# Kernel optimization log

Measured on AMD Instinct MI355X. Metric: run time of the kernel, lower is better.

Reference implementation:

```python
import jax, jax.numpy as jnp
import numpy as np

N_RAYS = 8192
M = 524288
GX, GY, GZ = 160, 160, 128
NFEAT = 12
POS_PE, VIEW_PE = 10, 4
WIDTH = 128
POS_DIM = 3 + 3 * POS_PE * 2      # 63
VIEW_DIM = 3 + 3 * VIEW_PE * 2    # 27
DIM0 = NFEAT + POS_DIM            # 75
ACT_SHIFT = float(np.log(1.0 / (1.0 - 1e-6) - 1.0))  # density bias shift from alpha_init
INTERVAL = 0.5                    # stepsize * voxel_size_ratio
XYZ_MIN, XYZ_MAX = -1.0, 1.0


def posemb(x, n_pe):
    # x: [N,3] -> [N, 3 + 3*n_pe*2], matching cat([x, sin(x*freq), cos(x*freq)])
    freq = 2.0 ** jnp.arange(n_pe, dtype=x.dtype)
    xf = (x[..., None] * freq).reshape(x.shape[0], -1)
    return jnp.concatenate([x, jnp.sin(xf), jnp.cos(xf)], axis=-1)


def trilinear(grid, xyz):
    # grid: [X,Y,Z,C]; xyz: [M,3] in world coords. align_corners=True bilinear (grid_sample).
    sz_f = jnp.array(grid.shape[:3], jnp.float32)
    sz_i = jnp.array(grid.shape[:3], jnp.int32)
    t = (xyz - XYZ_MIN) / (XYZ_MAX - XYZ_MIN) * (sz_f - 1.0)
    t = jnp.clip(t, 0.0, sz_f - 1.0)
    i0 = jnp.clip(jnp.floor(t).astype(jnp.int32), 0, sz_i - 2)
    f = t - i0.astype(t.dtype)
    out = jnp.zeros((xyz.shape[0], grid.shape[-1]), t.dtype)
    for dx in (0, 1):
        for dy in (0, 1):
            for dz in (0, 1):
                w = ((f[:, 0] if dx else 1.0 - f[:, 0])
                     * (f[:, 1] if dy else 1.0 - f[:, 1])
                     * (f[:, 2] if dz else 1.0 - f[:, 2]))
                out = out + w[:, None] * grid[i0[:, 0] + dx, i0[:, 1] + dy, i0[:, 2] + dz]
    return out


def mask_lookup(mask, xyz):
    # nearest-neighbor maskcache_lookup: ijk = round(xyz*scale + shift)
    sz_f = jnp.array(mask.shape, jnp.float32)
    scale = (sz_f - 1.0) / (XYZ_MAX - XYZ_MIN)
    shift = -XYZ_MIN * scale
    ijk = jnp.clip(jnp.round(xyz * scale + shift).astype(jnp.int32), 0,
                   jnp.array(mask.shape, jnp.int32) - 1)
    return mask[ijk[:, 0], ijk[:, 1], ijk[:, 2]]


def alphas2weights(alpha, ray_id, n_rays):
    # segmented T_i = prod_{j<i in ray}(1-alpha_j); weights = T*alpha (ray_id sorted)
    log1a = jnp.log(jnp.clip(1.0 - alpha, 1e-10, 1.0))
    excl = jnp.cumsum(log1a) - log1a                      # global exclusive cumsum
    seg_tot = jax.ops.segment_sum(log1a, ray_id, num_segments=n_rays)
    seg_start = jnp.cumsum(seg_tot) - seg_tot             # exclusive prefix over rays
    T = jnp.exp(excl - seg_start[ray_id])
    weights = T * alpha
    alphainv_last = jnp.exp(seg_tot)
    return weights, alphainv_last


def setup_inputs() -> dict:
    key = jax.random.key(0)
    ks = jax.random.split(key, 16)
    xyz = jax.random.uniform(ks[0], (M, 3), jnp.float32) * (XYZ_MAX - XYZ_MIN) + XYZ_MIN
    ray_id = jnp.sort(jax.random.randint(ks[1], (M,), 0, N_RAYS))
    viewdirs = jax.random.normal(ks[2], (N_RAYS, 3), jnp.float32)
    viewdirs = viewdirs / jnp.linalg.norm(viewdirs, axis=-1, keepdims=True)
    mask = jax.random.uniform(ks[3], (GX, GY, GZ)) > 0.1
    density = jax.random.normal(ks[4], (GX, GY, GZ), jnp.float32) * 0.5
    k0 = jax.random.normal(ks[5], (GX, GY, GZ, NFEAT), jnp.float32) * 0.1
    s = 0.05
    W0 = jax.random.normal(ks[6], (DIM0, WIDTH), jnp.float32) * s
    b0 = jnp.zeros((WIDTH,), jnp.float32)
    W1 = jax.random.normal(ks[7], (WIDTH, WIDTH), jnp.float32) * s
    b1 = jnp.zeros((WIDTH,), jnp.float32)
    W2 = jax.random.normal(ks[8], (WIDTH, WIDTH), jnp.float32) * s
    b2 = jnp.zeros((WIDTH,), jnp.float32)
    Wr = jax.random.normal(ks[9], (WIDTH + VIEW_DIM, 3), jnp.float32) * s
    br = jnp.zeros((3,), jnp.float32)
    return {"xyz": xyz, "ray_id": ray_id, "viewdirs": viewdirs, "mask": mask,
            "density": density, "k0": k0, "W0": W0, "b0": b0, "W1": W1, "b1": b1,
            "W2": W2, "b2": b2, "Wr": Wr, "br": br}


def reference(xyz, ray_id, viewdirs, mask, density, k0, W0, b0, W1, b1, W2, b2, Wr, br):
    # 1) empty-space skipping via mask cache (kept as multiplicative mask for static shapes)
    m = mask_lookup(mask, xyz).astype(xyz.dtype)
    # 2) trilinear density query + raw2alpha
    d = trilinear(density[..., None], xyz)[:, 0]
    alpha = 1.0 - (1.0 + jnp.exp(d + ACT_SHIFT)) ** (-INTERVAL)
    alpha = alpha * m
    # 3) segmented alpha compositing (Alphas2Weights)
    weights, alphainv_last = alphas2weights(alpha, ray_id, N_RAYS)
    # 4) feature query + view MLP -> rgb
    feat = trilinear(k0, xyz)                              # [M, NFEAT]
    h = jnp.concatenate([feat, posemb(xyz, POS_PE)], -1)   # [M, DIM0]
    h = jax.nn.relu(h @ W0 + b0)
    h = jax.nn.relu(h @ W1 + b1)
    h = jax.nn.relu(h @ W2 + b2)
    ve = posemb(viewdirs, VIEW_PE)[ray_id]                 # [M, VIEW_DIM]
    rgb = jax.nn.sigmoid(jnp.concatenate([h, ve], -1) @ Wr + br)
    # 5) composite per ray + white background
    rgb_marched = jax.ops.segment_sum(weights[:, None] * rgb, ray_id, num_segments=N_RAYS)
    rgb_marched = rgb_marched + alphainv_last[:, None] * 1.0
    return rgb_marched
```

## Files before the change

### kernel.cpp

```cpp
#include <hip/hip_runtime.h>
#include <hip/hip_bf16.h>

#define M_SAMPLES 524288
#define NRAYS 8192
#define GXD 160
#define GYD 160
#define GZD 128
#define GYZ (GYD*GZD)
#define NVOX (GXD*GYD*GZD)
#define ACT_SHIFT -13.81550955796f
#define ROWA 136
#define ROWB 168

typedef __bf16 bf16x8 __attribute__((ext_vector_type(8)));
typedef float f32x4 __attribute__((ext_vector_type(4)));
typedef float f32x16 __attribute__((ext_vector_type(16)));

static __device__ inline unsigned short f2bf(float f){
  __hip_bfloat16 h = __float2bfloat16(f);
  unsigned short u; __builtin_memcpy(&u, &h, 2); return u;
}

#if defined(__has_builtin)
#if __has_builtin(__builtin_amdgcn_cvt_pk_bf16_f32)
#define HAVE_PK_BF16 1
#endif
#endif

static __device__ inline unsigned int packbf(float a, float b){
#ifdef HAVE_PK_BF16
  typedef __bf16 bf16v2 __attribute__((ext_vector_type(2)));
  bf16v2 r = __builtin_amdgcn_cvt_pk_bf16_f32(a, b);
  unsigned int u; __builtin_memcpy(&u, &r, 4); return u;
#else
  return (unsigned int)f2bf(a) | ((unsigned int)f2bf(b) << 16);
#endif
}

struct Tri {
  int ix, iy, iz;
  float wx0, wx1, wy0, wy1, wz0, wz1;
};
static __device__ inline Tri tri_setup(float x, float y, float z){
  Tri t;
  float tx = (x+1.f)*0.5f*(float)(GXD-1); tx = fminf(fmaxf(tx,0.f),(float)(GXD-1));
  float ty = (y+1.f)*0.5f*(float)(GYD-1); ty = fminf(fmaxf(ty,0.f),(float)(GYD-1));
  float tz = (z+1.f)*0.5f*(float)(GZD-1); tz = fminf(fmaxf(tz,0.f),(float)(GZD-1));
  t.ix = min((int)tx, GXD-2); t.iy = min((int)ty, GYD-2); t.iz = min((int)tz, GZD-2);
  float fx = tx-t.ix, fy = ty-t.iy, fz = tz-t.iz;
  t.wx0 = 1.f-fx; t.wx1 = fx; t.wy0 = 1.f-fy; t.wy1 = fy; t.wz0 = 1.f-fz; t.wz1 = fz;
  return t;
}

__global__ void k_detect(const unsigned int* __restrict__ mw, int* __restrict__ flag){
  unsigned int v = mw[threadIdx.x & 63];
  unsigned long long any = __ballot(v > 1u);
  if(threadIdx.x == 0) *flag = (any != 0ull) ? 1 : 0;
}

__global__ __launch_bounds__(256) void k_prep_w(const float* __restrict__ W0,
    const float* __restrict__ W1, const float* __restrict__ W2,
    const float* __restrict__ Wr,
    unsigned short* __restrict__ wt0, unsigned short* __restrict__ wt1,
    unsigned short* __restrict__ wt2, unsigned short* __restrict__ wtr)
{
  int t = blockIdx.x*256 + threadIdx.x;
  if(t < 128*96){
    int n = t/96, k = t%96;
    wt0[t] = f2bf((k < 75) ? W0[k*128 + n] : 0.f);
  } else if(t < 128*96 + 16384){
    int j = t - 128*96; int n = j/128, k = j%128;
    wt1[j] = f2bf(W1[k*128 + n]);
  } else if(t < 128*96 + 32768){
    int j = t - 128*96 - 16384; int n = j/128, k = j%128;
    wt2[j] = f2bf(W2[k*128 + n]);
  } else if(t < 128*96 + 32768 + 16*160){
    int j = t - 128*96 - 32768; int n = j/160, k = j%160;
    wtr[j] = f2bf((n < 3 && k < 155) ? Wr[k*3 + n] : 0.f);
  }
}

__global__ __launch_bounds__(256) void k_viewemb(const float* __restrict__ vd,
                                                 float* __restrict__ ve)
{
  int t = blockIdx.x*256 + threadIdx.x;
  if(t >= NRAYS*27) return;
  int ray = t/27, c = t%27;
  float v;
  if(c < 3) v = vd[ray*3 + c];
  else if(c < 15){
    int q = c - 3; int ci = q/4, p = q%4;
    v = sinf(vd[ray*3 + ci] * (float)(1 << p));
  } else {
    int q = c - 15; int ci = q/4, p = q%4;
    v = cosf(vd[ray*3 + ci] * (float)(1 << p));
  }
  ve[t] = v;
}

template<int KDIM, int SROW, int DROW>
static __device__ inline void layer32(const unsigned short* src, unsigned short* dst,
    const unsigned short* __restrict__ wt, const float* __restrict__ bias,
    int wave, int ln, int kh)
{
  constexpr int NS = KDIM/16;
  int tile_s = wave & 1, tile_n = wave >> 1;
  const unsigned short* wbase = wt + (tile_n*32 + ln)*KDIM + kh*8;
  const unsigned short* abase = src + (tile_s*32 + ln)*SROW + kh*8;
  f32x16 acc = {0.f,0.f,0.f,0.f,0.f,0.f,0.f,0.f,0.f,0.f,0.f,0.f,0.f,0.f,0.f,0.f};
  #pragma unroll
  for(int st = 0; st < NS; ++st){
    bf16x8 af = *(const bf16x8*)(wbase + st*16);
    bf16x8 bfr = *(const bf16x8*)(abase + st*16);
    acc = __builtin_amdgcn_mfma_f32_32x32x16_bf16(af, bfr, acc, 0, 0, 0);
  }
  int scol = tile_s*32 + ln;
  #pragma unroll
  for(int g = 0; g < 4; ++g){
    int n0 = tile_n*32 + g*8 + kh*4;
    float4 bv = *(const float4*)(bias + n0);
    unsigned int lo = packbf(fmaxf(acc[4*g+0] + bv.x, 0.f), fmaxf(acc[4*g+1] + bv.y, 0.f));
    unsigned int hi = packbf(fmaxf(acc[4*g+2] + bv.z, 0.f), fmaxf(acc[4*g+3] + bv.w, 0.f));
    unsigned long long o = (unsigned long long)lo | ((unsigned long long)hi << 32);
    *(unsigned long long*)(dst + scol*DROW + n0) = o;
  }
}

__global__ __launch_bounds__(512) void k_mlp(const float* __restrict__ xyz,
    const float* __restrict__ density, const float* __restrict__ k0,
    const void* __restrict__ mask, const int* __restrict__ flag,
    const int* __restrict__ ray_id,
    const unsigned short* __restrict__ wt0, const unsigned short* __restrict__ wt1,
    const unsigned short* __restrict__ wt2, const unsigned short* __restrict__ wtr,
    const float* __restrict__ b0, const float* __restrict__ b1,
    const float* __restrict__ b2, const float* __restrict__ br,
    const float* __restrict__ ve,
    float* __restrict__ alpha_w, float4* __restrict__ rgb_out)
{
  __shared__ alignas(16) unsigned short hA[64*ROWA];
  __shared__ alignas(16) unsigned short hB[64*ROWB];
  __shared__ float red[64][4];

  int tid = threadIdx.x;
  int lane = tid & 63, wave = tid >> 6;

  if(wave < 4){
    int smp = (wave << 4) | (lane >> 2);
    int corner = lane & 3;
    int i = blockIdx.x*64 + smp;
    float x = xyz[3*i+0], y = xyz[3*i+1], z = xyz[3*i+2];
    Tri t = tri_setup(x, y, z);
    int dx = corner & 1, dy = corner >> 1;
    float wxy = (dx ? t.wx1 : t.wx0) * (dy ? t.wy1 : t.wy0);
    float w0 = wxy*t.wz0, w1 = wxy*t.wz1;
    size_t vox = (size_t)((t.ix+dx)*GYZ + (t.iy+dy)*GZD + t.iz);
    float pd = w0*density[vox] + w1*density[vox+1];
    const float4* v = (const float4*)(k0 + vox*12);
    float4 a0 = v[0], a1 = v[1], a2 = v[2];
    float4 c0 = v[3], c1 = v[4], c2 = v[5];
    float pf[12];
    pf[0] = w0*a0.x + w1*c0.x;  pf[1] = w0*a0.y + w1*c0.y;
    pf[2] = w0*a0.z + w1*c0.z;  pf[3] = w0*a0.w + w1*c0.w;
    pf[4] = w0*a1.x + w1*c1.x;  pf[5] = w0*a1.y + w1*c1.y;
    pf[6] = w0*a1.z + w1*c1.z;  pf[7] = w0*a1.w + w1*c1.w;
    pf[8] = w0*a2.x + w1*c2.x;  pf[9] = w0*a2.y + w1*c2.y;
    pf[10]= w0*a2.z + w1*c2.z;  pf[11]= w0*a2.w + w1*c2.w;
    #pragma unroll
    for(int m2 = 1; m2 < 4; m2 <<= 1){
      pd += __shfl_xor(pd, m2);
      #pragma unroll
      for(int j = 0; j < 12; ++j) pf[j] += __shfl_xor(pf[j], m2);
    }
    if(corner == 0){
      int mx = (int)rintf(x*79.5f + 79.5f); mx = min(max(mx,0), GXD-1);
      int my = (int)rintf(y*79.5f + 79.5f); my = min(max(my,0), GYD-1);
      int mz = (int)rintf(z*63.5f + 63.5f); mz = min(max(mz,0), GZD-1);
      int midx = mx*GYZ + my*GZD + mz;
      bool mm = (*flag) ? (((const unsigned char*)mask)[midx] != 0)
                        : (((const int*)mask)[midx] != 0);
      float e = expf(pd + ACT_SHIFT);
      float alpha = 1.f - rsqrtf(1.f + e);
      if(!mm) alpha = 0.f;
      alpha_w[i] = alpha;
      unsigned int d[8];
      #pragma unroll
      for(int j = 0; j < 6; ++j) d[j] = packbf(pf[2*j], pf[2*j+1]);
      d[6] = packbf(x, y);
      d[7] = packbf(z, __sinf(x));
      uint4* p = (uint4*)(hA + smp*ROWA);
      p[0] = make_uint4(d[0],d[1],d[2],d[3]);
      p[1] = make_uint4(d[4],d[5],d[6],d[7]);
    } else if(corner == 1){
      uint4* p = (uint4*)(hA + smp*ROWA + 80);
      p[0] = make_uint4(0,0,0,0);
      p[1] = make_uint4(0,0,0,0);
    } else {
      int ray = ray_id[i];
      int cb = (corner - 2) * 16;
      unsigned int d[8];
      #pragma unroll
      for(int j = 0; j < 8; ++j){
        int c = cb + 2*j;
        float a = (c     < 27) ? ve[ray*27 + c]     : 0.f;
        float b = (c + 1 < 27) ? ve[ray*27 + c + 1] : 0.f;
        d[j] = packbf(a, b);
      }
      uint4* p = (uint4*)(hB + smp*ROWB + 128 + cb);
      p[0] = make_uint4(d[0],d[1],d[2],d[3]);
      p[1] = make_uint4(d[4],d[5],d[6],d[7]);
    }
  } else {
    int chunk = wave - 3;
    int i2 = blockIdx.x*64 + lane;
    float x = xyz[3*i2+0], y = xyz[3*i2+1], z = xyz[3*i2+2];
    float vv[16];
    #pragma unroll
    for(int j = 0; j < 16; ++j){
      int c = chunk*16 + j;
      float r;
      if(c >= 75) r = 0.f;
      else {
        int q = (c < 45) ? (c-15) : (c-45);
        int ci = q/10, p = q - ci*10;
        float xv = (ci == 0) ? x : ((ci == 1) ? y : z);
        float a = xv * (float)(1 << p);
        r = (c < 45) ? __sinf(a) : __cosf(a);
      }
      vv[j] = r;
    }
    unsigned int d[8];
    #pragma unroll
    for(int j = 0; j < 8; ++j) d[j] = packbf(vv[2*j], vv[2*j+1]);
    uint4* p = (uint4*)(hA + lane*ROWA + chunk*16);
    p[0] = make_uint4(d[0],d[1],d[2],d[3]);
    p[1] = make_uint4(d[4],d[5],d[6],d[7]);
  }
  __syncthreads();

  int ln = lane & 31, kh = lane >> 5;
  layer32< 96, ROWA, ROWB>(hA, hB, wt0, b0, wave, ln, kh);  __syncthreads();
  layer32<128, ROWB, ROWA>(hB, hA, wt1, b1, wave, ln, kh);  __syncthreads();
  layer32<128, ROWA, ROWB>(hA, hB, wt2, b2, wave, ln, kh);  __syncthreads();

  int col = lane & 15, q = lane >> 4;
  if(wave < 4){
    int mt = wave;
    f32x4 acc = {0.f, 0.f, 0.f, 0.f};
    const unsigned short* arow = hB + (mt*16 + col)*ROWB + q*8;
    const unsigned short* wrow = wtr + col*160 + q*8;
    #pragma unroll
    for(int ks = 0; ks < 5; ++ks){
      bf16x8 af = *(const bf16x8*)(arow + ks*32);
      bf16x8 bfr = *(const bf16x8*)(wrow + ks*32);
      acc = __builtin_amdgcn_mfma_f32_16x16x32_bf16(af, bfr, acc, 0, 0, 0);
    }
    if(col < 3){
      #pragma unroll
      for(int r = 0; r < 4; ++r){
        int sl = mt*16 + q*4 + r;
        float v = acc[r] + br[col];
        red[sl][col] = 1.f / (1.f + expf(-v));
      }
    }
  }
  __syncthreads();

  if(wave == 7){
    int i2 = blockIdx.x*64 + lane;
    rgb_out[i2] = make_float4(red[lane][0], red[lane][1], red[lane][2], 0.f);
  }
}

__global__ __launch_bounds__(256) void k_comp2(const int* __restrict__ ray_id,
    const float* __restrict__ alpha_w, const float4* __restrict__ rgb,
    float* __restrict__ out)
{
  int r = blockIdx.x*4 + (threadIdx.x >> 6);
  int lane = threadIdx.x & 63;
  int lo = 0, hi = M_SAMPLES;
  while(lo < hi){ int mid = (lo+hi) >> 1; if(ray_id[mid] < r) lo = mid+1; else hi = mid; }
  int s = lo;
  int lo2 = s, hi2 = M_SAMPLES;
  while(lo2 < hi2){ int mid = (lo2+hi2) >> 1; if(ray_id[mid] < r+1) lo2 = mid+1; else hi2 = mid; }
  int e = lo2;

  float carry = 1.f;
  float ar = 0.f, ag = 0.f, ab = 0.f;
  for(int base = s; base < e; base += 64){
    int idx = base + lane;
    float a = (idx < e) ? alpha_w[idx] : 0.f;
    float incl = 1.f - a;
    #pragma unroll
    for(int d2 = 1; d2 < 64; d2 <<= 1){
      float t = __shfl_up(incl, d2);
      if(lane >= d2) incl *= t;
    }
    float excl = __shfl_up(incl, 1);
    if(lane == 0) excl = 1.f;
    float w = carry * excl * a;
    if(idx < e){
      float4 c = rgb[idx];
      ar += w*c.x; ag += w*c.y; ab += w*c.z;
    }
    carry *= __shfl(incl, 63);
  }
  #pragma unroll
  for(int m2 = 1; m2 < 64; m2 <<= 1){
    ar += __shfl_xor(ar, m2);
    ag += __shfl_xor(ag, m2);
    ab += __shfl_xor(ab, m2);
  }
  if(lane == 0){
    out[3*r+0] = ar + carry;
    out[3*r+1] = ag + carry;
    out[3*r+2] = ab + carry;
  }
}

extern "C" void kernel_launch(void* const* d_in, const int* in_sizes, int n_in,
                              void* d_out, int out_size, void* d_ws, size_t ws_size,
                              hipStream_t stream)
{
  const float* xyz      = (const float*)d_in[0];
  const int*   ray_id   = (const int*)  d_in[1];
  const float* viewdirs = (const float*)d_in[2];
  const void*  mask     =               d_in[3];
  const float* density  = (const float*)d_in[4];
  const float* k0       = (const float*)d_in[5];
  const float* W0 = (const float*)d_in[6];  const float* b0 = (const float*)d_in[7];
  const float* W1 = (const float*)d_in[8];  const float* b1 = (const float*)d_in[9];
  const float* W2 = (const float*)d_in[10]; const float* b2 = (const float*)d_in[11];
  const float* Wr = (const float*)d_in[12]; const float* br = (const float*)d_in[13];
  float* out = (float*)d_out;

  char* ws = (char*)d_ws;
  size_t off = 0;
  auto take = [&](size_t nbytes) -> void* {
    void* p = ws + off;
    off = (off + nbytes + 255) & ~(size_t)255;
    return p;
  };
  int*            flag    = (int*)           take(4);
  unsigned short* wt0     = (unsigned short*)take(128*96*2);
  unsigned short* wt1     = (unsigned short*)take(128*128*2);
  unsigned short* wt2     = (unsigned short*)take(128*128*2);
  unsigned short* wtr     = (unsigned short*)take(16*160*2);
  float*          ve      = (float*)         take((size_t)NRAYS*27*4);
  float*          alpha_w = (float*)         take((size_t)M_SAMPLES*4);
  float4*         rgb_ws  = (float4*)        take((size_t)M_SAMPLES*16);

  k_detect <<<1,   64,  0, stream>>>((const unsigned int*)mask, flag);
  k_prep_w <<<186, 256, 0, stream>>>(W0, W1, W2, Wr, wt0, wt1, wt2, wtr);
  k_viewemb<<<864, 256, 0, stream>>>(viewdirs, ve);
  k_mlp    <<<M_SAMPLES/64, 512, 0, stream>>>(xyz, density, k0, mask, flag,
                                              ray_id, wt0, wt1, wt2, wtr,
                                              b0, b1, b2, br, ve, alpha_w, rgb_ws);
  k_comp2  <<<NRAYS/4, 256, 0, stream>>>(ray_id, alpha_w, rgb_ws, out);
}
```

Before: 488.8 us.

## Repack density and k0 grids into compact FP8 voxel records and merge prep kernels

Adds a per-call repack kernel that interleaves density (fp32) with the 12 k0 features, stored as FP8 in one 16-byte record per voxel (bf16 in 32 bytes as a fallback). The MLP kernel then gathers two packed records per corner instead of separate density and 48-byte feature reads, cutting gather traffic. It also merges the detect, weight-prep and view-embedding kernels into one launch. The trade-off is an extra full-grid pass over roughly 3.3M voxels on every call, and FP8 feature quantization that may exceed tolerance.

```diff
diff --git a/kernel.cpp b/kernel.cpp
--- a/kernel.cpp
+++ b/kernel.cpp
@@ -15,15 +15,21 @@
 typedef __bf16 bf16x8 __attribute__((ext_vector_type(8)));
 typedef float f32x4 __attribute__((ext_vector_type(4)));
 typedef float f32x16 __attribute__((ext_vector_type(16)));
+typedef float f32v2 __attribute__((ext_vector_type(2)));
 
 static __device__ inline unsigned short f2bf(float f){
   __hip_bfloat16 h = __float2bfloat16(f);
   unsigned short u; __builtin_memcpy(&u, &h, 2); return u;
 }
+static __device__ inline float flo(unsigned int u){ return __uint_as_float(u << 16); }
+static __device__ inline float fhi(unsigned int u){ return __uint_as_float(u & 0xffff0000u); }
 
 #if defined(__has_builtin)
 #if __has_builtin(__builtin_amdgcn_cvt_pk_bf16_f32)
 #define HAVE_PK_BF16 1
+#endif
+#if __has_builtin(__builtin_amdgcn_cvt_pk_f32_fp8) && __has_builtin(__builtin_amdgcn_cvt_pk_fp8_f32)
+#define HAVE_FP8 1
 #endif
 #endif
 
@@ -52,38 +58,39 @@
   return t;
 }
 
-__global__ void k_detect(const unsigned int* __restrict__ mw, int* __restrict__ flag){
-  unsigned int v = mw[threadIdx.x & 63];
-  unsigned long long any = __ballot(v > 1u);
-  if(threadIdx.x == 0) *flag = (any != 0ull) ? 1 : 0;
-}
-
-__global__ __launch_bounds__(256) void k_prep_w(const float* __restrict__ W0,
-    const float* __restrict__ W1, const float* __restrict__ W2,
-    const float* __restrict__ Wr,
+__global__ __launch_bounds__(256) void k_prep(const unsigned int* __restrict__ mw,
+    int* __restrict__ flag,
+    const float* __restrict__ W0, const float* __restrict__ W1,
+    const float* __restrict__ W2, const float* __restrict__ Wr,
     unsigned short* __restrict__ wt0, unsigned short* __restrict__ wt1,
-    unsigned short* __restrict__ wt2, unsigned short* __restrict__ wtr)
-{
-  int t = blockIdx.x*256 + threadIdx.x;
-  if(t < 128*96){
-    int n = t/96, k = t%96;
-    wt0[t] = f2bf((k < 75) ? W0[k*128 + n] : 0.f);
-  } else if(t < 128*96 + 16384){
-    int j = t - 128*96; int n = j/128, k = j%128;
-    wt1[j] = f2bf(W1[k*128 + n]);
-  } else if(t < 128*96 + 32768){
-    int j = t - 128*96 - 16384; int n = j/128, k = j%128;
-    wt2[j] = f2bf(W2[k*128 + n]);
-  } else if(t < 128*96 + 32768 + 16*160){
-    int j = t - 128*96 - 32768; int n = j/160, k = j%160;
-    wtr[j] = f2bf((n < 3 && k < 155) ? Wr[k*3 + n] : 0.f);
-  }
-}
-
-__global__ __launch_bounds__(256) void k_viewemb(const float* __restrict__ vd,
-                                                 float* __restrict__ ve)
-{
-  int t = blockIdx.x*256 + threadIdx.x;
+    unsigned short* __restrict__ wt2, unsigned short* __restrict__ wtr,
+    const float* __restrict__ vd, float* __restrict__ ve)
+{
+  int b = blockIdx.x;
+  if(b == 0){
+    unsigned int v = mw[threadIdx.x & 63];
+    unsigned long long any = __ballot(v > 1u);
+    if(threadIdx.x == 0) *flag = (any != 0ull) ? 1 : 0;
+    return;
+  }
+  if(b < 187){
+    int t = (b-1)*256 + threadIdx.x;
+    if(t < 128*96){
+      int n = t/96, k = t%96;
+      wt0[t] = f2bf((k < 75) ? W0[k*128 + n] : 0.f);
+    } else if(t < 128*96 + 16384){
+      int j = t - 128*96; int n = j/128, k = j%128;
+      wt1[j] = f2bf(W1[k*128 + n]);
+    } else if(t < 128*96 + 32768){
+      int j = t - 128*96 - 16384; int n = j/128, k = j%128;
+      wt2[j] = f2bf(W2[k*128 + n]);
+    } else if(t < 128*96 + 32768 + 16*160){
+      int j = t - 128*96 - 32768; int n = j/160, k = j%160;
+      wtr[j] = f2bf((n < 3 && k < 155) ? Wr[k*3 + n] : 0.f);
+    }
+    return;
+  }
+  int t = (b-187)*256 + threadIdx.x;
   if(t >= NRAYS*27) return;
   int ray = t/27, c = t%27;
   float v;
@@ -98,6 +105,46 @@
   ve[t] = v;
 }
 
+#ifdef HAVE_FP8
+__global__ __launch_bounds__(256) void k_repack(const float* __restrict__ density,
+    const float* __restrict__ k0, uint4* __restrict__ packed)
+{
+  int v = blockIdx.x*256 + threadIdx.x;
+  if(v >= NVOX) return;
+  const float4* kp = (const float4*)(k0 + (size_t)v*12);
+  float4 a = kp[0], b = kp[1], c = kp[2];
+  uint4 o;
+  o.x = __float_as_uint(density[v]);
+  int w;
+  w = __builtin_amdgcn_cvt_pk_fp8_f32(a.x, a.y, 0, false);
+  w = __builtin_amdgcn_cvt_pk_fp8_f32(a.z, a.w, w, true);
+  o.y = (unsigned int)w;
+  w = __builtin_amdgcn_cvt_pk_fp8_f32(b.x, b.y, 0, false);
+  w = __builtin_amdgcn_cvt_pk_fp8_f32(b.z, b.w, w, true);
+  o.z = (unsigned int)w;
+  w = __builtin_amdgcn_cvt_pk_fp8_f32(c.x, c.y, 0, false);
+  w = __builtin_amdgcn_cvt_pk_fp8_f32(c.z, c.w, w, true);
+  o.w = (unsigned int)w;
+  packed[v] = o;
+}
+#else
+__global__ __launch_bounds__(256) void k_repack(const float* __restrict__ density,
+    const float* __restrict__ k0, uint4* __restrict__ packed)
+{
+  int v = blockIdx.x*256 + threadIdx.x;
+  if(v >= NVOX) return;
+  const float4* kp = (const float4*)(k0 + (size_t)v*12);
+  float4 a = kp[0], b = kp[1], c = kp[2];
+  uint4 o0, o1;
+  o0.x = __float_as_uint(density[v]);
+  o0.y = packbf(a.x, a.y); o0.z = packbf(a.z, a.w); o0.w = packbf(b.x, b.y);
+  o1.x = packbf(b.z, b.w); o1.y = packbf(c.x, c.y); o1.z = packbf(c.z, c.w);
+  o1.w = 0;
+  packed[(size_t)v*2]   = o0;
+  packed[(size_t)v*2+1] = o1;
+}
+#endif
+
 template<int KDIM, int SROW, int DROW>
 static __device__ inline void layer32(const unsigned short* src, unsigned short* dst,
     const unsigned short* __restrict__ wt, const float* __restrict__ bias,
@@ -126,7 +173,9 @@
   }
 }
 
+template<int PACKED>
 __global__ __launch_bounds__(512) void k_mlp(const float* __restrict__ xyz,
+    const uint4* __restrict__ packed,
     const float* __restrict__ density, const float* __restrict__ k0,
     const void* __restrict__ mask, const int* __restrict__ flag,
     const int* __restrict__ ray_id,
@@ -154,17 +203,57 @@
     float wxy = (dx ? t.wx1 : t.wx0) * (dy ? t.wy1 : t.wy0);
     float w0 = wxy*t.wz0, w1 = wxy*t.wz1;
     size_t vox = (size_t)((t.ix+dx)*GYZ + (t.iy+dy)*GZD + t.iz);
-    float pd = w0*density[vox] + w1*density[vox+1];
-    const float4* v = (const float4*)(k0 + vox*12);
-    float4 a0 = v[0], a1 = v[1], a2 = v[2];
-    float4 c0 = v[3], c1 = v[4], c2 = v[5];
+    float pd;
     float pf[12];
-    pf[0] = w0*a0.x + w1*c0.x;  pf[1] = w0*a0.y + w1*c0.y;
-    pf[2] = w0*a0.z + w1*c0.z;  pf[3] = w0*a0.w + w1*c0.w;
-    pf[4] = w0*a1.x + w1*c1.x;  pf[5] = w0*a1.y + w1*c1.y;
-    pf[6] = w0*a1.z + w1*c1.z;  pf[7] = w0*a1.w + w1*c1.w;
-    pf[8] = w0*a2.x + w1*c2.x;  pf[9] = w0*a2.y + w1*c2.y;
-    pf[10]= w0*a2.z + w1*c2.z;  pf[11]= w0*a2.w + w1*c2.w;
+#ifdef HAVE_FP8
+    if(PACKED){
+      uint4 q0 = packed[vox], q1 = packed[vox+1];
+      pd = w0*__uint_as_float(q0.x) + w1*__uint_as_float(q1.x);
+      f32v2 a, b;
+      a = __builtin_amdgcn_cvt_pk_f32_fp8((int)q0.y, false);
+      b = __builtin_amdgcn_cvt_pk_f32_fp8((int)q1.y, false);
+      pf[0] = w0*a.x + w1*b.x;  pf[1] = w0*a.y + w1*b.y;
+      a = __builtin_amdgcn_cvt_pk_f32_fp8((int)q0.y, true);
+      b = __builtin_amdgcn_cvt_pk_f32_fp8((int)q1.y, true);
+      pf[2] = w0*a.x + w1*b.x;  pf[3] = w0*a.y + w1*b.y;
+      a = __builtin_amdgcn_cvt_pk_f32_fp8((int)q0.z, false);
+      b = __builtin_amdgcn_cvt_pk_f32_fp8((int)q1.z, false);
+      pf[4] = w0*a.x + w1*b.x;  pf[5] = w0*a.y + w1*b.y;
+      a = __builtin_amdgcn_cvt_pk_f32_fp8((int)q0.z, true);
+      b = __builtin_amdgcn_cvt_pk_f32_fp8((int)q1.z, true);
+      pf[6] = w0*a.x + w1*b.x;  pf[7] = w0*a.y + w1*b.y;
+      a = __builtin_amdgcn_cvt_pk_f32_fp8((int)q0.w, false);
+      b = __builtin_amdgcn_cvt_pk_f32_fp8((int)q1.w, false);
+      pf[8] = w0*a.x + w1*b.x;  pf[9] = w0*a.y + w1*b.y;
+      a = __builtin_amdgcn_cvt_pk_f32_fp8((int)q0.w, true);
+      b = __builtin_amdgcn_cvt_pk_f32_fp8((int)q1.w, true);
+      pf[10]= w0*a.x + w1*b.x;  pf[11]= w0*a.y + w1*b.y;
+    }
+#else
+    if(PACKED){
+      const uint4* pv = packed + vox*2;
+      uint4 q0 = pv[0], q1 = pv[1], q2 = pv[2], q3 = pv[3];
+      pd = w0*__uint_as_float(q0.x) + w1*__uint_as_float(q2.x);
+      pf[0]  = w0*flo(q0.y) + w1*flo(q2.y);  pf[1]  = w0*fhi(q0.y) + w1*fhi(q2.y);
+      pf[2]  = w0*flo(q0.z) + w1*flo(q2.z);  pf[3]  = w0*fhi(q0.z) + w1*fhi(q2.z);
+      pf[4]  = w0*flo(q0.w) + w1*flo(q2.w);  pf[5]  = w0*fhi(q0.w) + w1*fhi(q2.w);
+      pf[6]  = w0*flo(q1.x) + w1*flo(q3.x);  pf[7]  = w0*fhi(q1.x) + w1*fhi(q3.x);
+      pf[8]  = w0*flo(q1.y) + w1*flo(q3.y);  pf[9]  = w0*fhi(q1.y) + w1*fhi(q3.y);
+      pf[10] = w0*flo(q1.z) + w1*flo(q3.z);  pf[11] = w0*fhi(q1.z) + w1*fhi(q3.z);
+    }
+#endif
+    if(!PACKED){
+      pd = w0*density[vox] + w1*density[vox+1];
+      const float4* v = (const float4*)(k0 + vox*12);
+      float4 a0 = v[0], a1 = v[1], a2 = v[2];
+      float4 c0 = v[3], c1 = v[4], c2 = v[5];
+      pf[0] = w0*a0.x + w1*c0.x;  pf[1] = w0*a0.y + w1*c0.y;
+      pf[2] = w0*a0.z + w1*c0.z;  pf[3] = w0*a0.w + w1*c0.w;
+      pf[4] = w0*a1.x + w1*c1.x;  pf[5] = w0*a1.y + w1*c1.y;
+      pf[6] = w0*a1.z + w1*c1.z;  pf[7] = w0*a1.w + w1*c1.w;
+      pf[8] = w0*a2.x + w1*c2.x;  pf[9] = w0*a2.y + w1*c2.y;
+      pf[10]= w0*a2.z + w1*c2.z;  pf[11]= w0*a2.w + w1*c2.w;
+    }
     #pragma unroll
     for(int m2 = 1; m2 < 4; m2 <<= 1){
       pd += __shfl_xor(pd, m2);
@@ -348,12 +437,24 @@
   float*          ve      = (float*)         take((size_t)NRAYS*27*4);
   float*          alpha_w = (float*)         take((size_t)M_SAMPLES*4);
   float4*         rgb_ws  = (float4*)        take((size_t)M_SAMPLES*16);
-
-  k_detect <<<1,   64,  0, stream>>>((const unsigned int*)mask, flag);
-  k_prep_w <<<186, 256, 0, stream>>>(W0, W1, W2, Wr, wt0, wt1, wt2, wtr);
-  k_viewemb<<<864, 256, 0, stream>>>(viewdirs, ve);
-  k_mlp    <<<M_SAMPLES/64, 512, 0, stream>>>(xyz, density, k0, mask, flag,
-                                              ray_id, wt0, wt1, wt2, wtr,
-                                              b0, b1, b2, br, ve, alpha_w, rgb_ws);
-  k_comp2  <<<NRAYS/4, 256, 0, stream>>>(ray_id, alpha_w, rgb_ws, out);
-}
+#ifdef HAVE_FP8
+  uint4*          packed  = (uint4*)         take((size_t)NVOX*16);
+#else
+  uint4*          packed  = (uint4*)         take((size_t)NVOX*32);
+#endif
+  bool use_packed = (ws_size >= off);
+
+  k_prep<<<1051, 256, 0, stream>>>((const unsigned int*)mask, flag,
+                                   W0, W1, W2, Wr, wt0, wt1, wt2, wtr, viewdirs, ve);
+  if(use_packed){
+    k_repack<<<(NVOX+255)/256, 256, 0, stream>>>(density, k0, packed);
+    k_mlp<1><<<M_SAMPLES/64, 512, 0, stream>>>(xyz, packed, density, k0, mask, flag,
+                                               ray_id, wt0, wt1, wt2, wtr,
+                                               b0, b1, b2, br, ve, alpha_w, rgb_ws);
+  } else {
+    k_mlp<0><<<M_SAMPLES/64, 512, 0, stream>>>(xyz, packed, density, k0, mask, flag,
+                                               ray_id, wt0, wt1, wt2, wtr,
+                                               b0, b1, b2, br, ve, alpha_w, rgb_ws);
+  }
+  k_comp2<<<NRAYS/4, 256, 0, stream>>>(ray_id, alpha_w, rgb_ws, out);
+}
```

New measurement: 486.9 us. No clear change (-0.4%).
